# Optimization experiments

Hardware: AMD Instinct MI355X
Metric: run time of the kernel (lower is better)

## Reference

```python
import jax, jax.numpy as jnp
import numpy as np

B, S, D, L, INNER = 16, 512, 768, 20, 64
NEG = 1e12


def setup_inputs() -> dict:
    key = jax.random.key(0)
    k1, k2, k3 = jax.random.split(key, 3)
    x = jax.random.normal(k1, (B, S, D), jnp.float32)
    attention_mask = jnp.ones((B, S), jnp.int32)
    w1 = jax.random.normal(k2, (D, 2 * INNER), jnp.float32) * 0.02
    b1 = jnp.zeros((2 * INNER,), jnp.float32)
    w2 = jax.random.normal(k3, (D, 2 * L), jnp.float32) * 0.02
    b2 = jnp.zeros((2 * L,), jnp.float32)
    return {"x": x, "attention_mask": attention_mask, "w1": w1, "b1": b1, "w2": w2, "b2": b2}


def _rope(v, cos_pos, sin_pos):
    # interleaved rotation: [-v1, v0, -v3, v2, ...]
    v2 = jnp.stack([-v[..., 1::2], v[..., ::2]], axis=-1).reshape(v.shape)
    return v * cos_pos + v2 * sin_pos


def reference(x, attention_mask, w1, b1, w2, b2):
    Bc, Sc, _ = x.shape
    out1 = x @ w1 + b1                       # [B,S,2*INNER]
    qw, kw = out1[..., ::2], out1[..., 1::2]  # each [B,S,INNER]
    # sinusoidal position embedding, interleaved sin/cos -> [1,S,INNER]
    pos_ids = jnp.arange(Sc, dtype=jnp.float32)[:, None]
    idx = jnp.arange(INNER // 2, dtype=jnp.float32)
    freqs = jnp.power(10000.0, -2.0 * idx / INNER)
    ang = pos_ids * freqs                    # [S, INNER//2]
    pos = jnp.stack([jnp.sin(ang), jnp.cos(ang)], axis=-1).reshape(1, Sc, INNER)
    cos_pos = jnp.repeat(pos[..., 1::2], 2, axis=-1)
    sin_pos = jnp.repeat(pos[..., ::2], 2, axis=-1)
    qw = _rope(qw, cos_pos, sin_pos)
    kw = _rope(kw, cos_pos, sin_pos)
    logits = jnp.einsum('bmd,bnd->bmn', qw, kw) / jnp.sqrt(jnp.float32(INNER))  # [B,S,S]
    dense = jnp.swapaxes(x @ w2 + b2, 1, 2) / 2.0  # [B,2L,S]
    # broadcast per-label start/end biases -> [B,L,S,S]
    logits = logits[:, None] + dense[:, ::2, None, :] + dense[:, 1::2, :, None]
    m = attention_mask.astype(logits.dtype)
    m1 = m[:, None, :, None]
    m2 = m[:, None, None, :]
    logits = logits * m1 - NEG * (1.0 - m1)
    logits = logits * m2 - NEG * (1.0 - m2)
    tril = jnp.tril(jnp.ones((Sc, Sc), logits.dtype), -1)
    logits = logits - tril * NEG
    probs = jax.nn.sigmoid(logits)
    return logits, probs
```

## Files before the change

kernel.cpp:

```cpp
#include <hip/hip_runtime.h>

typedef float v4 __attribute__((ext_vector_type(4)));
typedef float v2 __attribute__((ext_vector_type(2)));

#define NEGV 1000000000000.0f
#define SEQ 512
#define NB 16
#define NL 20
#define LOGITS_ELEMS (16 * 20 * 512 * 512)

__global__ __launch_bounds__(256)
void prep_kernel(const float* __restrict__ x, const float* __restrict__ w1,
                 const float* __restrict__ b1, const float* __restrict__ w2,
                 const float* __restrict__ b2,
                 float* __restrict__ qw, float* __restrict__ kw,
                 float* __restrict__ dense)
{
    __shared__ float xs[32][36];
    __shared__ float wsm[32][64];

    const int tid = threadIdx.x;
    const int jb = blockIdx.x;
    const int m0 = blockIdx.y * 32;
    const int j0 = jb * 64;

    const int tx = tid & 15;
    const int ty = tid >> 4;

    const int sxm = tid >> 3;
    const int sxk = (tid & 7) * 4;
    const int swk = tid >> 3;
    const int swn = (tid & 7) * 8;

    float acc0[4] = {0.f, 0.f, 0.f, 0.f};
    float acc1[4] = {0.f, 0.f, 0.f, 0.f};

    for (int k0 = 0; k0 < 768; k0 += 32) {
        v4 xa = *(const v4*)&x[(size_t)(m0 + sxm) * 768 + k0 + sxk];
        v4 wa, wb;
        if (jb < 2) {
            wa = *(const v4*)&w1[(size_t)(k0 + swk) * 128 + j0 + swn];
            wb = *(const v4*)&w1[(size_t)(k0 + swk) * 128 + j0 + swn + 4];
        } else if (swn < 40) {
            wa = *(const v4*)&w2[(size_t)(k0 + swk) * 40 + swn];
            wb = *(const v4*)&w2[(size_t)(k0 + swk) * 40 + swn + 4];
        } else {
            wa = 0.0f; wb = 0.0f;
        }
        __syncthreads();
        *(v4*)&xs[sxm][sxk] = xa;
        *(v4*)&wsm[swk][swn] = wa;
        *(v4*)&wsm[swk][swn + 4] = wb;
        __syncthreads();
#pragma unroll
        for (int k = 0; k < 32; k += 4) {
            v4 a0 = *(const v4*)&xs[ty][k];
            v4 a1 = *(const v4*)&xs[ty + 16][k];
            v4 bv0 = *(const v4*)&wsm[k + 0][tx * 4];
            v4 bv1 = *(const v4*)&wsm[k + 1][tx * 4];
            v4 bv2 = *(const v4*)&wsm[k + 2][tx * 4];
            v4 bv3 = *(const v4*)&wsm[k + 3][tx * 4];
#pragma unroll
            for (int j = 0; j < 4; ++j) {
                acc0[j] += a0[0] * bv0[j] + a0[1] * bv1[j] + a0[2] * bv2[j] + a0[3] * bv3[j];
                acc1[j] += a1[0] * bv0[j] + a1[1] * bv1[j] + a1[2] * bv2[j] + a1[3] * bv3[j];
            }
        }
    }

    if (jb < 2) {
        const int p = (j0 >> 2) + tx;
        const float fr = __powf(10000.0f, (float)(-2 * p) / 64.0f);
        v4 bb = *(const v4*)&b1[j0 + tx * 4];
#pragma unroll
        for (int i = 0; i < 2; ++i) {
            const float* acc = (i == 0) ? acc0 : acc1;
            const int mrow = m0 + ty + 16 * i;
            const int s = mrow & 511;
            float ang = (float)s * fr;
            float sn = sinf(ang), cs = cosf(ang);
            float q0 = acc[0] + bb[0];
            float k0v = acc[1] + bb[1];
            float q1 = acc[2] + bb[2];
            float k1v = acc[3] + bb[3];
            v2 qo, ko;
            qo[0] = q0 * cs - q1 * sn;  qo[1] = q1 * cs + q0 * sn;
            ko[0] = k0v * cs - k1v * sn; ko[1] = k1v * cs + k0v * sn;
            *(v2*)&qw[(size_t)mrow * 64 + 2 * p] = qo;
            *(v2*)&kw[(size_t)mrow * 64 + 2 * p] = ko;
        }
    } else if (tx < 10) {
        v4 bb = *(const v4*)&b2[tx * 4];
#pragma unroll
        for (int i = 0; i < 2; ++i) {
            const float* acc = (i == 0) ? acc0 : acc1;
            const int mrow = m0 + ty + 16 * i;
            const int bi = mrow >> 9;
            const int s = mrow & 511;
#pragma unroll
            for (int j = 0; j < 4; ++j) {
                dense[(size_t)(bi * 40 + tx * 4 + j) * 512 + s] = (acc[j] + bb[j]) * 0.5f;
            }
        }
    }
}

__global__ __launch_bounds__(256)
void fused_kernel(const float* __restrict__ qw, const float* __restrict__ kw,
                  const float* __restrict__ dense, const int* __restrict__ mask,
                  float* __restrict__ outL, float* __restrict__ outP)
{
    __shared__ float qwL[32][68];
    __shared__ float kwT[64][64];
    __shared__ float dEs[20][64];
    __shared__ float dOs[20][32];
    __shared__ float mMs[32];
    __shared__ float mNs[64];

    const int tid = threadIdx.x;
    const int n0 = blockIdx.x * 64;
    const int m0 = blockIdx.y * 32;
    const int b  = blockIdx.z;

    {
        const int m = tid >> 3, kk = (tid & 7) * 8;
        v4 a = *(const v4*)&qw[(size_t)(b * SEQ + m0 + m) * 64 + kk];
        v4 c = *(const v4*)&qw[(size_t)(b * SEQ + m0 + m) * 64 + kk + 4];
        *(v4*)&qwL[m][kk] = a;
        *(v4*)&qwL[m][kk + 4] = c;
    }
    {
        const int n = tid >> 2, kk = (tid & 3) * 16;
#pragma unroll
        for (int t = 0; t < 4; ++t) {
            v4 a = *(const v4*)&kw[(size_t)(b * SEQ + n0 + n) * 64 + kk + 4 * t];
            kwT[kk + 4 * t + 0][n] = a[0];
            kwT[kk + 4 * t + 1][n] = a[1];
            kwT[kk + 4 * t + 2][n] = a[2];
            kwT[kk + 4 * t + 3][n] = a[3];
        }
    }
#pragma unroll
    for (int t = 0; t < 5; ++t) {
        int flat = t * 256 + tid;
        int l = flat >> 6, n = flat & 63;
        dEs[l][n] = dense[(size_t)(b * 40 + 2 * l) * 512 + n0 + n];
    }
#pragma unroll
    for (int t = 0; t < 3; ++t) {
        int flat = t * 256 + tid;
        if (flat < 640) {
            int l = flat >> 5, m = flat & 31;
            dOs[l][m] = dense[(size_t)(b * 40 + 2 * l + 1) * 512 + m0 + m];
        }
    }
    if (tid < 64) mNs[tid] = (float)mask[b * SEQ + n0 + tid];
    else if (tid < 96) mMs[tid - 64] = (float)mask[b * SEQ + m0 + (tid - 64)];
    __syncthreads();

    const int tx = tid & 15;
    const int r  = tid >> 4;

    float acc0[4] = {0.f, 0.f, 0.f, 0.f};
    float acc1[4] = {0.f, 0.f, 0.f, 0.f};
#pragma unroll
    for (int k = 0; k < 64; k += 4) {
        v4 a0 = *(const v4*)&qwL[r][k];
        v4 a1 = *(const v4*)&qwL[r + 16][k];
        v4 bv0 = *(const v4*)&kwT[k + 0][tx * 4];
        v4 bv1 = *(const v4*)&kwT[k + 1][tx * 4];
        v4 bv2 = *(const v4*)&kwT[k + 2][tx * 4];
        v4 bv3 = *(const v4*)&kwT[k + 3][tx * 4];
#pragma unroll
        for (int j = 0; j < 4; ++j) {
            acc0[j] += a0[0] * bv0[j] + a0[1] * bv1[j] + a0[2] * bv2[j] + a0[3] * bv3[j];
            acc1[j] += a1[0] * bv0[j] + a1[1] * bv1[j] + a1[2] * bv2[j] + a1[3] * bv3[j];
        }
    }

    const float mM0 = mMs[r], mM1 = mMs[r + 16];
    const float cM0 = -NEGV * (1.0f - mM0);
    const float cM1 = -NEGV * (1.0f - mM1);
    v4 mNv = *(const v4*)&mNs[tx * 4];
    v4 cN;
#pragma unroll
    for (int j = 0; j < 4; ++j) cN[j] = -NEGV * (1.0f - mNv[j]);
    const int gm0 = m0 + r, gm1 = m0 + r + 16;
#pragma unroll
    for (int j = 0; j < 4; ++j) { acc0[j] *= 0.125f; acc1[j] *= 0.125f; }

    for (int l = 0; l < NL; ++l) {
        v4 de = *(const v4*)&dEs[l][tx * 4];
        float do0 = dOs[l][r], do1 = dOs[l][r + 16];
        v4 lv0, lv1, pv0, pv1;
#pragma unroll
        for (int j = 0; j < 4; ++j) {
            const int gn = n0 + tx * 4 + j;
            float v = acc0[j] + de[j] + do0;
            v = v * mM0 + cM0;
            v = v * mNv[j] + cN[j];
            if (gm0 > gn) v -= NEGV;
            lv0[j] = v;
            pv0[j] = __builtin_amdgcn_rcpf(1.0f + __expf(-v));
            float u = acc1[j] + de[j] + do1;
            u = u * mM1 + cM1;
            u = u * mNv[j] + cN[j];
            if (gm1 > gn) u -= NEGV;
            lv1[j] = u;
            pv1[j] = __builtin_amdgcn_rcpf(1.0f + __expf(-u));
        }
        const size_t base0 = ((size_t)(b * NL + l) * SEQ + gm0) * SEQ + n0 + tx * 4;
        const size_t base1 = ((size_t)(b * NL + l) * SEQ + gm1) * SEQ + n0 + tx * 4;
        *(v4*)&outL[base0] = lv0;
        *(v4*)&outL[base1] = lv1;
        *(v4*)&outP[base0] = pv0;
        *(v4*)&outP[base1] = pv1;
    }
}

extern "C" void kernel_launch(void* const* d_in, const int* in_sizes, int n_in,
                              void* d_out, int out_size, void* d_ws, size_t ws_size,
                              hipStream_t stream) {
    (void)in_sizes; (void)n_in; (void)out_size; (void)ws_size;
    const float* x    = (const float*)d_in[0];
    const int*   mask = (const int*)d_in[1];
    const float* w1   = (const float*)d_in[2];
    const float* b1   = (const float*)d_in[3];
    const float* w2   = (const float*)d_in[4];
    const float* b2   = (const float*)d_in[5];

    float* ws = (float*)d_ws;
    float* qw    = ws;
    float* kw    = ws + 524288;
    float* dense = ws + 1048576;

    float* outL = (float*)d_out;
    float* outP = outL + (size_t)LOGITS_ELEMS;

    prep_kernel<<<dim3(3, 256), 256, 0, stream>>>(x, w1, b1, w2, b2, qw, kw, dense);
    fused_kernel<<<dim3(8, 16, 16), 256, 0, stream>>>(qw, kw, dense, mask, outL, outP);
}
```

Before: 734.4 us.

## Compute full QK row stripe per block and stream coalesced nontemporal output stores

The fused kernel now assigns one block per 32-row stripe of a batch. It computes all 512 QK columns into a large shared-memory tile, then writes each output row contiguously across the block with nontemporal stores. Dense and mask values are read straight from global memory per column. The prep GEMM uses 128 threads with a 4x4 register tile per thread. The aim is wider coalesced writes and less redundant staging, at the cost of far fewer blocks and heavy LDS use, which limits occupancy.

```diff
diff --git a/kernel.cpp b/kernel.cpp
--- a/kernel.cpp
+++ b/kernel.cpp
@@ -2,14 +2,14 @@
 
 typedef float v4 __attribute__((ext_vector_type(4)));
 typedef float v2 __attribute__((ext_vector_type(2)));
+typedef int  iv4 __attribute__((ext_vector_type(4)));
 
 #define NEGV 1000000000000.0f
 #define SEQ 512
-#define NB 16
 #define NL 20
 #define LOGITS_ELEMS (16 * 20 * 512 * 512)
 
-__global__ __launch_bounds__(256)
+__global__ __launch_bounds__(128)
 void prep_kernel(const float* __restrict__ x, const float* __restrict__ w1,
                  const float* __restrict__ b1, const float* __restrict__ w2,
                  const float* __restrict__ b2,
@@ -27,43 +27,51 @@
     const int tx = tid & 15;
     const int ty = tid >> 4;
 
-    const int sxm = tid >> 3;
-    const int sxk = (tid & 7) * 4;
-    const int swk = tid >> 3;
-    const int swn = (tid & 7) * 8;
-
-    float acc0[4] = {0.f, 0.f, 0.f, 0.f};
-    float acc1[4] = {0.f, 0.f, 0.f, 0.f};
+    const int sxm = tid >> 2;
+    const int sxk = (tid & 3) * 8;
+    const int swk = tid >> 2;
+    const int swn = (tid & 3) * 16;
+
+    float acc[4][4] = {};
 
     for (int k0 = 0; k0 < 768; k0 += 32) {
         v4 xa = *(const v4*)&x[(size_t)(m0 + sxm) * 768 + k0 + sxk];
-        v4 wa, wb;
+        v4 xb = *(const v4*)&x[(size_t)(m0 + sxm) * 768 + k0 + sxk + 4];
+        v4 wv[4];
         if (jb < 2) {
-            wa = *(const v4*)&w1[(size_t)(k0 + swk) * 128 + j0 + swn];
-            wb = *(const v4*)&w1[(size_t)(k0 + swk) * 128 + j0 + swn + 4];
-        } else if (swn < 40) {
-            wa = *(const v4*)&w2[(size_t)(k0 + swk) * 40 + swn];
-            wb = *(const v4*)&w2[(size_t)(k0 + swk) * 40 + swn + 4];
+            const float* wp = &w1[(size_t)(k0 + swk) * 128 + j0 + swn];
+#pragma unroll
+            for (int t = 0; t < 4; ++t) wv[t] = *(const v4*)(wp + 4 * t);
         } else {
-            wa = 0.0f; wb = 0.0f;
+            const float* wp = &w2[(size_t)(k0 + swk) * 40 + swn];
+#pragma unroll
+            for (int t = 0; t < 4; ++t) {
+                if (swn + 4 * t < 40) wv[t] = *(const v4*)(wp + 4 * t);
+                else                  wv[t] = 0.0f;
+            }
         }
         __syncthreads();
         *(v4*)&xs[sxm][sxk] = xa;
-        *(v4*)&wsm[swk][swn] = wa;
-        *(v4*)&wsm[swk][swn + 4] = wb;
+        *(v4*)&xs[sxm][sxk + 4] = xb;
+#pragma unroll
+        for (int t = 0; t < 4; ++t) *(v4*)&wsm[swk][swn + 4 * t] = wv[t];
         __syncthreads();
 #pragma unroll
         for (int k = 0; k < 32; k += 4) {
-            v4 a0 = *(const v4*)&xs[ty][k];
-            v4 a1 = *(const v4*)&xs[ty + 16][k];
-            v4 bv0 = *(const v4*)&wsm[k + 0][tx * 4];
-            v4 bv1 = *(const v4*)&wsm[k + 1][tx * 4];
-            v4 bv2 = *(const v4*)&wsm[k + 2][tx * 4];
-            v4 bv3 = *(const v4*)&wsm[k + 3][tx * 4];
-#pragma unroll
-            for (int j = 0; j < 4; ++j) {
-                acc0[j] += a0[0] * bv0[j] + a0[1] * bv1[j] + a0[2] * bv2[j] + a0[3] * bv3[j];
-                acc1[j] += a1[0] * bv0[j] + a1[1] * bv1[j] + a1[2] * bv2[j] + a1[3] * bv3[j];
+            v4 a0 = *(const v4*)&xs[4 * ty + 0][k];
+            v4 a1 = *(const v4*)&xs[4 * ty + 1][k];
+            v4 a2 = *(const v4*)&xs[4 * ty + 2][k];
+            v4 a3 = *(const v4*)&xs[4 * ty + 3][k];
+            v4 b0v = *(const v4*)&wsm[k + 0][tx * 4];
+            v4 b1v = *(const v4*)&wsm[k + 1][tx * 4];
+            v4 b2v = *(const v4*)&wsm[k + 2][tx * 4];
+            v4 b3v = *(const v4*)&wsm[k + 3][tx * 4];
+#pragma unroll
+            for (int j = 0; j < 4; ++j) {
+                acc[0][j] += a0[0] * b0v[j] + a0[1] * b1v[j] + a0[2] * b2v[j] + a0[3] * b3v[j];
+                acc[1][j] += a1[0] * b0v[j] + a1[1] * b1v[j] + a1[2] * b2v[j] + a1[3] * b3v[j];
+                acc[2][j] += a2[0] * b0v[j] + a2[1] * b1v[j] + a2[2] * b2v[j] + a2[3] * b3v[j];
+                acc[3][j] += a3[0] * b0v[j] + a3[1] * b1v[j] + a3[2] * b2v[j] + a3[3] * b3v[j];
             }
         }
     }
@@ -73,18 +81,17 @@
         const float fr = __powf(10000.0f, (float)(-2 * p) / 64.0f);
         v4 bb = *(const v4*)&b1[j0 + tx * 4];
 #pragma unroll
-        for (int i = 0; i < 2; ++i) {
-            const float* acc = (i == 0) ? acc0 : acc1;
-            const int mrow = m0 + ty + 16 * i;
+        for (int i = 0; i < 4; ++i) {
+            const int mrow = m0 + 4 * ty + i;
             const int s = mrow & 511;
             float ang = (float)s * fr;
             float sn = sinf(ang), cs = cosf(ang);
-            float q0 = acc[0] + bb[0];
-            float k0v = acc[1] + bb[1];
-            float q1 = acc[2] + bb[2];
-            float k1v = acc[3] + bb[3];
+            float q0  = acc[i][0] + bb[0];
+            float k0v = acc[i][1] + bb[1];
+            float q1  = acc[i][2] + bb[2];
+            float k1v = acc[i][3] + bb[3];
             v2 qo, ko;
-            qo[0] = q0 * cs - q1 * sn;  qo[1] = q1 * cs + q0 * sn;
+            qo[0] = q0 * cs - q1 * sn;   qo[1] = q1 * cs + q0 * sn;
             ko[0] = k0v * cs - k1v * sn; ko[1] = k1v * cs + k0v * sn;
             *(v2*)&qw[(size_t)mrow * 64 + 2 * p] = qo;
             *(v2*)&kw[(size_t)mrow * 64 + 2 * p] = ko;
@@ -92,14 +99,13 @@
     } else if (tx < 10) {
         v4 bb = *(const v4*)&b2[tx * 4];
 #pragma unroll
-        for (int i = 0; i < 2; ++i) {
-            const float* acc = (i == 0) ? acc0 : acc1;
-            const int mrow = m0 + ty + 16 * i;
+        for (int i = 0; i < 4; ++i) {
+            const int mrow = m0 + 4 * ty + i;
             const int bi = mrow >> 9;
             const int s = mrow & 511;
 #pragma unroll
             for (int j = 0; j < 4; ++j) {
-                dense[(size_t)(bi * 40 + tx * 4 + j) * 512 + s] = (acc[j] + bb[j]) * 0.5f;
+                dense[(size_t)(bi * 40 + tx * 4 + j) * 512 + s] = (acc[i][j] + bb[j]) * 0.5f;
             }
         }
     }
@@ -110,17 +116,15 @@
                   const float* __restrict__ dense, const int* __restrict__ mask,
                   float* __restrict__ outL, float* __restrict__ outP)
 {
+    __shared__ float qkS[32][516];
     __shared__ float qwL[32][68];
     __shared__ float kwT[64][64];
-    __shared__ float dEs[20][64];
     __shared__ float dOs[20][32];
     __shared__ float mMs[32];
-    __shared__ float mNs[64];
 
     const int tid = threadIdx.x;
-    const int n0 = blockIdx.x * 64;
-    const int m0 = blockIdx.y * 32;
-    const int b  = blockIdx.z;
+    const int m0 = blockIdx.x * 32;
+    const int b  = blockIdx.y;
 
     {
         const int m = tid >> 3, kk = (tid & 7) * 8;
@@ -129,23 +133,6 @@
         *(v4*)&qwL[m][kk] = a;
         *(v4*)&qwL[m][kk + 4] = c;
     }
-    {
-        const int n = tid >> 2, kk = (tid & 3) * 16;
-#pragma unroll
-        for (int t = 0; t < 4; ++t) {
-            v4 a = *(const v4*)&kw[(size_t)(b * SEQ + n0 + n) * 64 + kk + 4 * t];
-            kwT[kk + 4 * t + 0][n] = a[0];
-            kwT[kk + 4 * t + 1][n] = a[1];
-            kwT[kk + 4 * t + 2][n] = a[2];
-            kwT[kk + 4 * t + 3][n] = a[3];
-        }
-    }
-#pragma unroll
-    for (int t = 0; t < 5; ++t) {
-        int flat = t * 256 + tid;
-        int l = flat >> 6, n = flat & 63;
-        dEs[l][n] = dense[(size_t)(b * 40 + 2 * l) * 512 + n0 + n];
-    }
 #pragma unroll
     for (int t = 0; t < 3; ++t) {
         int flat = t * 256 + tid;
@@ -154,67 +141,90 @@
             dOs[l][m] = dense[(size_t)(b * 40 + 2 * l + 1) * 512 + m0 + m];
         }
     }
-    if (tid < 64) mNs[tid] = (float)mask[b * SEQ + n0 + tid];
-    else if (tid < 96) mMs[tid - 64] = (float)mask[b * SEQ + m0 + (tid - 64)];
+    if (tid < 32) mMs[tid] = (float)mask[b * SEQ + m0 + tid];
+
+    const int txc = tid & 15;
+    const int r   = tid >> 4;
+    const int kn  = tid >> 2;
+    const int kkk = (tid & 3) * 16;
+
+    for (int nc = 0; nc < 8; ++nc) {
+        const int n0 = nc * 64;
+        v4 kv[4];
+#pragma unroll
+        for (int t = 0; t < 4; ++t)
+            kv[t] = *(const v4*)&kw[(size_t)(b * SEQ + n0 + kn) * 64 + kkk + 4 * t];
+        __syncthreads();
+#pragma unroll
+        for (int t = 0; t < 4; ++t) {
+            kwT[kkk + 4 * t + 0][kn] = kv[t][0];
+            kwT[kkk + 4 * t + 1][kn] = kv[t][1];
+            kwT[kkk + 4 * t + 2][kn] = kv[t][2];
+            kwT[kkk + 4 * t + 3][kn] = kv[t][3];
+        }
+        __syncthreads();
+
+        float acc0[4] = {0.f, 0.f, 0.f, 0.f};
+        float acc1[4] = {0.f, 0.f, 0.f, 0.f};
+#pragma unroll
+        for (int k = 0; k < 64; k += 4) {
+            v4 a0 = *(const v4*)&qwL[r][k];
+            v4 a1 = *(const v4*)&qwL[r + 16][k];
+            v4 bv0 = *(const v4*)&kwT[k + 0][txc * 4];
+            v4 bv1 = *(const v4*)&kwT[k + 1][txc * 4];
+            v4 bv2 = *(const v4*)&kwT[k + 2][txc * 4];
+            v4 bv3 = *(const v4*)&kwT[k + 3][txc * 4];
+#pragma unroll
+            for (int j = 0; j < 4; ++j) {
+                acc0[j] += a0[0] * bv0[j] + a0[1] * bv1[j] + a0[2] * bv2[j] + a0[3] * bv3[j];
+                acc1[j] += a1[0] * bv0[j] + a1[1] * bv1[j] + a1[2] * bv2[j] + a1[3] * bv3[j];
+            }
+        }
+        v4 o0, o1;
+#pragma unroll
+        for (int j = 0; j < 4; ++j) { o0[j] = acc0[j] * 0.125f; o1[j] = acc1[j] * 0.125f; }
+        *(v4*)&qkS[r][n0 + txc * 4] = o0;
+        *(v4*)&qkS[r + 16][n0 + txc * 4] = o1;
+    }
     __syncthreads();
 
-    const int tx = tid & 15;
-    const int r  = tid >> 4;
-
-    float acc0[4] = {0.f, 0.f, 0.f, 0.f};
-    float acc1[4] = {0.f, 0.f, 0.f, 0.f};
-#pragma unroll
-    for (int k = 0; k < 64; k += 4) {
-        v4 a0 = *(const v4*)&qwL[r][k];
-        v4 a1 = *(const v4*)&qwL[r + 16][k];
-        v4 bv0 = *(const v4*)&kwT[k + 0][tx * 4];
-        v4 bv1 = *(const v4*)&kwT[k + 1][tx * 4];
-        v4 bv2 = *(const v4*)&kwT[k + 2][tx * 4];
-        v4 bv3 = *(const v4*)&kwT[k + 3][tx * 4];
-#pragma unroll
-        for (int j = 0; j < 4; ++j) {
-            acc0[j] += a0[0] * bv0[j] + a0[1] * bv1[j] + a0[2] * bv2[j] + a0[3] * bv3[j];
-            acc1[j] += a1[0] * bv0[j] + a1[1] * bv1[j] + a1[2] * bv2[j] + a1[3] * bv3[j];
-        }
-    }
-
-    const float mM0 = mMs[r], mM1 = mMs[r + 16];
-    const float cM0 = -NEGV * (1.0f - mM0);
-    const float cM1 = -NEGV * (1.0f - mM1);
-    v4 mNv = *(const v4*)&mNs[tx * 4];
-    v4 cN;
-#pragma unroll
-    for (int j = 0; j < 4; ++j) cN[j] = -NEGV * (1.0f - mNv[j]);
-    const int gm0 = m0 + r, gm1 = m0 + r + 16;
-#pragma unroll
-    for (int j = 0; j < 4; ++j) { acc0[j] *= 0.125f; acc1[j] *= 0.125f; }
+    const int c    = tid & 127;
+    const int half = tid >> 7;
+    const int gn0  = c * 4;
+
+    iv4 mi = *(const iv4*)&mask[b * SEQ + gn0];
+    v4 mNv, cN;
+#pragma unroll
+    for (int j = 0; j < 4; ++j) {
+        mNv[j] = (float)mi[j];
+        cN[j] = -NEGV * (1.0f - mNv[j]);
+    }
 
     for (int l = 0; l < NL; ++l) {
-        v4 de = *(const v4*)&dEs[l][tx * 4];
-        float do0 = dOs[l][r], do1 = dOs[l][r + 16];
-        v4 lv0, lv1, pv0, pv1;
-#pragma unroll
-        for (int j = 0; j < 4; ++j) {
-            const int gn = n0 + tx * 4 + j;
-            float v = acc0[j] + de[j] + do0;
-            v = v * mM0 + cM0;
-            v = v * mNv[j] + cN[j];
-            if (gm0 > gn) v -= NEGV;
-            lv0[j] = v;
-            pv0[j] = __builtin_amdgcn_rcpf(1.0f + __expf(-v));
-            float u = acc1[j] + de[j] + do1;
-            u = u * mM1 + cM1;
-            u = u * mNv[j] + cN[j];
-            if (gm1 > gn) u -= NEGV;
-            lv1[j] = u;
-            pv1[j] = __builtin_amdgcn_rcpf(1.0f + __expf(-u));
-        }
-        const size_t base0 = ((size_t)(b * NL + l) * SEQ + gm0) * SEQ + n0 + tx * 4;
-        const size_t base1 = ((size_t)(b * NL + l) * SEQ + gm1) * SEQ + n0 + tx * 4;
-        *(v4*)&outL[base0] = lv0;
-        *(v4*)&outL[base1] = lv1;
-        *(v4*)&outP[base0] = pv0;
-        *(v4*)&outP[base1] = pv1;
+        v4 de = *(const v4*)&dense[(size_t)(b * 40 + 2 * l) * 512 + gn0];
+        const size_t lbase = ((size_t)(b * NL + l) * SEQ + m0) * SEQ + gn0;
+#pragma unroll
+        for (int it = 0; it < 16; ++it) {
+            const int row  = it * 2 + half;
+            const int grow = m0 + row;
+            v4 qk = *(const v4*)&qkS[row][gn0];
+            const float doo = dOs[l][row];
+            const float mM  = mMs[row];
+            const float cM  = -NEGV * (1.0f - mM);
+            v4 lv, pv;
+#pragma unroll
+            for (int j = 0; j < 4; ++j) {
+                float v = qk[j] + de[j] + doo;
+                v = v * mM + cM;
+                v = v * mNv[j] + cN[j];
+                if (grow > gn0 + j) v -= NEGV;
+                lv[j] = v;
+                pv[j] = __builtin_amdgcn_rcpf(1.0f + __expf(-v));
+            }
+            const size_t base = lbase + (size_t)row * SEQ;
+            __builtin_nontemporal_store(lv, (v4*)&outL[base]);
+            __builtin_nontemporal_store(pv, (v4*)&outP[base]);
+        }
     }
 }
 
@@ -237,6 +247,6 @@
     float* outL = (float*)d_out;
     float* outP = outL + (size_t)LOGITS_ELEMS;
 
-    prep_kernel<<<dim3(3, 256), 256, 0, stream>>>(x, w1, b1, w2, b2, qw, kw, dense);
-    fused_kernel<<<dim3(8, 16, 16), 256, 0, stream>>>(qw, kw, dense, mask, outL, outP);
+    prep_kernel<<<dim3(3, 256), 128, 0, stream>>>(x, w1, b1, w2, b2, qw, kw, dense);
+    fused_kernel<<<dim3(16, 16), 256, 0, stream>>>(qw, kw, dense, mask, outL, outP);
 }
```

After: 761.8 us. 3.7% more time.
